# Kernel optimization log

Measured on AMD Instinct MI355X. Metric: run time of the kernel, lower is better.

The kernel has to match this reference:

```python
import jax, jax.numpy as jnp
import numpy as np

NA, NH, E, EL, D = 100000, 20000, 1000000, 200000, 128


def _sage(x_src, x_dst, src, dst, W_l, b_l, W_r, num_dst):
    # PyG SAGEConv: out = lin_l(mean_j x_src[j]) + lin_r(x_dst); lin_l has bias, lin_r does not.
    msg = x_src[src]                                   # [E, D] gather
    agg = jax.ops.segment_sum(msg, dst, num_segments=num_dst)   # [num_dst, D]
    deg = jax.ops.segment_sum(jnp.ones((src.shape[0],), x_src.dtype), dst, num_segments=num_dst)
    agg = agg / jnp.maximum(deg, 1.0)[:, None]         # mean aggregation; isolated nodes -> 0
    return agg @ W_l + b_l + x_dst @ W_r


def setup_inputs() -> dict:
    key = jax.random.key(0)
    ks = jax.random.split(key, 24)
    s = 1.0 / np.sqrt(D)
    inp = {
        "x_author": jax.random.normal(ks[0], (NA, D), jnp.float32),
        "x_hotel": jax.random.normal(ks[1], (NH, D), jnp.float32),
        "ei_ah_src": jax.random.randint(ks[2], (E,), 0, NA, jnp.int32),
        "ei_ah_dst": jax.random.randint(ks[3], (E,), 0, NH, jnp.int32),
        "ei_ha_src": jax.random.randint(ks[4], (E,), 0, NH, jnp.int32),
        "ei_ha_dst": jax.random.randint(ks[5], (E,), 0, NA, jnp.int32),
        "eli_row": jax.random.randint(ks[6], (EL,), 0, NA, jnp.int32),
        "eli_col": jax.random.randint(ks[7], (EL,), 0, NH, jnp.int32),
    }
    # per-layer, per-edge-type SAGE weights
    names = ["W1_ah_l", "W1_ah_r", "W1_ha_l", "W1_ha_r", "W2_ah_l", "W2_ah_r", "W2_ha_l", "W2_ha_r"]
    for i, n in enumerate(names):
        inp[n] = jax.random.normal(ks[8 + i], (D, D), jnp.float32) * s
    inp["b1_ah_l"] = jnp.zeros((D,), jnp.float32)
    inp["b1_ha_l"] = jnp.zeros((D,), jnp.float32)
    inp["b2_ah_l"] = jnp.zeros((D,), jnp.float32)
    inp["b2_ha_l"] = jnp.zeros((D,), jnp.float32)
    # decoder MLP
    inp["W_lin1"] = jax.random.normal(ks[16], (2 * D, D), jnp.float32) * (1.0 / np.sqrt(2 * D))
    inp["b_lin1"] = jnp.zeros((D,), jnp.float32)
    inp["W_lin2"] = jax.random.normal(ks[17], (D, 1), jnp.float32) * s
    inp["b_lin2"] = jnp.zeros((1,), jnp.float32)
    return inp


def reference(x_author, x_hotel, ei_ah_src, ei_ah_dst, ei_ha_src, ei_ha_dst,
              eli_row, eli_col,
              W1_ah_l, b1_ah_l, W1_ah_r, W1_ha_l, b1_ha_l, W1_ha_r,
              W2_ah_l, b2_ah_l, W2_ah_r, W2_ha_l, b2_ha_l, W2_ha_r,
              W_lin1, b_lin1, W_lin2, b_lin2):
    # layer 1 (HeteroConv: each node type receives from exactly one edge type) + relu
    h_hotel = jax.nn.relu(_sage(x_author, x_hotel, ei_ah_src, ei_ah_dst, W1_ah_l, b1_ah_l, W1_ah_r, NH))
    h_author = jax.nn.relu(_sage(x_hotel, x_author, ei_ha_src, ei_ha_dst, W1_ha_l, b1_ha_l, W1_ha_r, NA))
    # layer 2 (no relu on last layer)
    z_hotel = _sage(h_author, h_hotel, ei_ah_src, ei_ah_dst, W2_ah_l, b2_ah_l, W2_ah_r, NH)
    z_author = _sage(h_hotel, h_author, ei_ha_src, ei_ha_dst, W2_ha_l, b2_ha_l, W2_ha_r, NA)
    # edge decoder: gather-concat -> 2-layer MLP
    z1 = jnp.concatenate([z_author[eli_row], z_hotel[eli_col]], axis=-1)  # [EL, 2D]
    z2 = jax.nn.relu(z1 @ W_lin1 + b_lin1)                                # [EL, D]
    pred = (z2 @ W_lin2 + b_lin2).reshape(-1)                             # [EL]
    return (pred, z1, z2)
```

## Files before the change

kernel.cpp:

```cpp
#include <hip/hip_runtime.h>

#define NA_ 100000
#define NH_ 20000
#define E_  1000000
#define EL_ 200000
#define D_  128

typedef __attribute__((ext_vector_type(8))) short short8;
typedef __attribute__((ext_vector_type(4))) float f32x4;

__device__ __forceinline__ ushort f2bf(float f) {
  union { float f; uint u; } v; v.f = f;
  uint u = v.u;
  return (ushort)((u + 0x7FFFu + ((u >> 16) & 1u)) >> 16);
}
__device__ __forceinline__ uint pack2bf(float a, float b) {
  return (uint)f2bf(a) | ((uint)f2bf(b) << 16);
}


__global__ __launch_bounds__(256) void cvt_count_k(const float* __restrict__ xa, ushort* __restrict__ da,
                                                   const float* __restrict__ xh, ushort* __restrict__ dh,
                                                   const int* __restrict__ d1, int* __restrict__ c1,
                                                   const int* __restrict__ d2, int* __restrict__ c2) {
  int i = blockIdx.x * 256 + threadIdx.x;
  if (i < E_) atomicAdd(&c1[d1[i]], 1);
  else if (i < 2 * E_) atomicAdd(&c2[d2[i - E_]], 1);
  const int na4 = NA_ * 32;
  if (i < na4) {
    float4 v = *(const float4*)(xa + (size_t)i * 4);
    ((uint2*)da)[i] = make_uint2(pack2bf(v.x, v.y), pack2bf(v.z, v.w));
  } else {
    int k = i - na4;
    if (k < NH_ * 32) {
      float4 v = *(const float4*)(xh + (size_t)k * 4);
      ((uint2*)dh)[k] = make_uint2(pack2bf(v.x, v.y), pack2bf(v.z, v.w));
    }
  }
}


__global__ __launch_bounds__(1024) void scan2_k(int* __restrict__ c1, int* __restrict__ o1, int n1,
                                                int* __restrict__ c2, int* __restrict__ o2, int n2) {
  int* c = blockIdx.x ? c2 : c1;
  int* o = blockIdx.x ? o2 : o1;
  int n  = blockIdx.x ? n2 : n1;
  __shared__ int sums[1024];
  int t = threadIdx.x;
  int per = (n + 1023) >> 10;
  int s0 = t * per;
  int s1 = s0 + per; if (s1 > n) s1 = n;
  int loc = 0;
  for (int i = s0; i < s1; i++) loc += c[i];
  sums[t] = loc;
  __syncthreads();
  for (int sh = 1; sh < 1024; sh <<= 1) {
    int v = (t >= sh) ? sums[t - sh] : 0;
    __syncthreads();
    sums[t] += v;
    __syncthreads();
  }
  int run = (t == 0) ? 0 : sums[t - 1];
  for (int i = s0; i < s1; i++) {
    int ci = c[i];
    o[i] = run;
    c[i] = run;
    run += ci;
  }
  if (t == 1023) o[n] = run;
}

__global__ void fill_edges_k(const int* __restrict__ s1, const int* __restrict__ d1,
                             int* __restrict__ cur1, int* __restrict__ out1,
                             const int* __restrict__ s2, const int* __restrict__ d2,
                             int* __restrict__ cur2, int* __restrict__ out2) {
  int i = blockIdx.x * 256 + threadIdx.x;
  if (i < E_) {
    int p = atomicAdd(&cur1[d1[i]], 1);
    out1[p] = s1[i];
  } else if (i < 2 * E_) {
    int ii = i - E_;
    int p = atomicAdd(&cur2[d2[ii]], 1);
    out2[p] = s2[ii];
  }
}


__global__ void pack_all_k(const float* a0, const float* a1, ushort* ad,
                           const float* b0, const float* b1, ushort* bd,
                           const float* c0, const float* c1, ushort* cd,
                           const float* d0, const float* d1, ushort* dd,
                           const float* e0, const float* e1, ushort* ed) {
  const float *s0, *s1; ushort* dst;
  switch (blockIdx.y) {
    case 0: s0 = a0; s1 = a1; dst = ad; break;
    case 1: s0 = b0; s1 = b1; dst = bd; break;
    case 2: s0 = c0; s1 = c1; dst = cd; break;
    case 3: s0 = d0; s1 = d1; dst = dd; break;
    default: s0 = e0; s1 = e1; dst = ed; break;
  }
  int idx = blockIdx.x * 256 + threadIdx.x;
  int j = idx & 7, lane = (idx >> 3) & 63, nt = (idx >> 9) & 7, kc = idx >> 12;
  int k = kc * 32 + (lane >> 4) * 8 + j;
  int n = nt * 16 + (lane & 15);
  float v = (k < 128) ? s0[k * 128 + n] : s1[(k - 128) * 128 + n];
  dst[idx] = f2bf(v);
}


__global__ __launch_bounds__(256) void aggregate_bf_k(const ushort* __restrict__ xsrc,
                                                      const int* __restrict__ off,
                                                      const int* __restrict__ srcs,
                                                      ushort* __restrict__ out, int ndst) {
  int w = (blockIdx.x * 256 + threadIdx.x) >> 6;
  int lane = threadIdx.x & 63;
  if (w >= ndst) return;
  const int grp = lane >> 4, sub = lane & 15;
  int beg = off[w], end = off[w + 1];
  float a[8] = {0.f, 0.f, 0.f, 0.f, 0.f, 0.f, 0.f, 0.f};
  const ushort* base = xsrc + sub * 8;
  int j = beg + grp;
  for (; j + 4 < end; j += 8) {
    int sA = srcs[j];
    int sB = srcs[j + 4];
    uint4 vA = *(const uint4*)(base + (size_t)sA * 128);
    uint4 vB = *(const uint4*)(base + (size_t)sB * 128);
    a[0] += __uint_as_float(vA.x << 16); a[1] += __uint_as_float(vA.x & 0xFFFF0000u);
    a[2] += __uint_as_float(vA.y << 16); a[3] += __uint_as_float(vA.y & 0xFFFF0000u);
    a[4] += __uint_as_float(vA.z << 16); a[5] += __uint_as_float(vA.z & 0xFFFF0000u);
    a[6] += __uint_as_float(vA.w << 16); a[7] += __uint_as_float(vA.w & 0xFFFF0000u);
    a[0] += __uint_as_float(vB.x << 16); a[1] += __uint_as_float(vB.x & 0xFFFF0000u);
    a[2] += __uint_as_float(vB.y << 16); a[3] += __uint_as_float(vB.y & 0xFFFF0000u);
    a[4] += __uint_as_float(vB.z << 16); a[5] += __uint_as_float(vB.z & 0xFFFF0000u);
    a[6] += __uint_as_float(vB.w << 16); a[7] += __uint_as_float(vB.w & 0xFFFF0000u);
  }
  if (j < end) {
    int sA = srcs[j];
    uint4 vA = *(const uint4*)(base + (size_t)sA * 128);
    a[0] += __uint_as_float(vA.x << 16); a[1] += __uint_as_float(vA.x & 0xFFFF0000u);
    a[2] += __uint_as_float(vA.y << 16); a[3] += __uint_as_float(vA.y & 0xFFFF0000u);
    a[4] += __uint_as_float(vA.z << 16); a[5] += __uint_as_float(vA.z & 0xFFFF0000u);
    a[6] += __uint_as_float(vA.w << 16); a[7] += __uint_as_float(vA.w & 0xFFFF0000u);
  }
#pragma unroll
  for (int k = 0; k < 8; k++) {
    a[k] += __shfl_xor(a[k], 16);
    a[k] += __shfl_xor(a[k], 32);
  }
  int deg = end - beg;
  float sc = 1.0f / (float)(deg > 0 ? deg : 1);
  if (grp == 0) {
    uint4 o;
    o.x = pack2bf(a[0] * sc, a[1] * sc);
    o.y = pack2bf(a[2] * sc, a[3] * sc);
    o.z = pack2bf(a[4] * sc, a[5] * sc);
    o.w = pack2bf(a[6] * sc, a[7] * sc);
    *(uint4*)(out + (size_t)w * 128 + sub * 8) = o;
  }
}


template <bool RELU, bool OUTBF>
__global__ __launch_bounds__(256) void sage_mfma_k(const ushort* __restrict__ Abf,
                                                   const ushort* __restrict__ Xbf,
                                                   const ushort* __restrict__ Wp,
                                                   const float* __restrict__ bias,
                                                   float* __restrict__ outF,
                                                   ushort* __restrict__ outB, int rows) {
  const int t = threadIdx.x;
  const int w = t >> 6, lane = t & 63, quad = lane >> 4, m = lane & 15;
  const int row0 = blockIdx.x * 64 + w * 16;
  int rA = row0 + m; if (rA >= rows) rA = rows - 1;
  f32x4 acc[8];
#pragma unroll
  for (int nt = 0; nt < 8; nt++) acc[nt] = (f32x4){0.f, 0.f, 0.f, 0.f};
#pragma unroll
  for (int kc = 0; kc < 8; kc++) {
    const ushort* src = (kc < 4) ? (Abf + (size_t)rA * 128 + kc * 32)
                                 : (Xbf + (size_t)rA * 128 + (kc - 4) * 32);
    short8 a = *(const short8*)(src + quad * 8);
    const ushort* wp = Wp + (size_t)(kc * 8) * 512 + lane * 8;
#pragma unroll
    for (int nt = 0; nt < 8; nt++) {
      short8 b = *(const short8*)(wp + nt * 512);
      acc[nt] = __builtin_amdgcn_mfma_f32_16x16x32_bf16(a, b, acc[nt], 0, 0, 0);
    }
  }
#pragma unroll
  for (int nt = 0; nt < 8; nt++) {
    float bv = bias[nt * 16 + m];
#pragma unroll
    for (int r = 0; r < 4; r++) {
      int row = row0 + quad * 4 + r;
      if (row < rows) {
        float v = acc[nt][r] + bv;
        if (RELU) v = fmaxf(v, 0.f);
        if (OUTBF) outB[(size_t)row * 128 + nt * 16 + m] = f2bf(v);
        else       outF[(size_t)row * 128 + nt * 16 + m] = v;
      }
    }
  }
}


__global__ __launch_bounds__(256) void decoder_mfma_k(const float* __restrict__ Za,
                                                      const float* __restrict__ Zh,
                                                      const int* __restrict__ rowi,
                                                      const int* __restrict__ coli,
                                                      const ushort* __restrict__ Wp,
                                                      const float* __restrict__ b1,
                                                      const float* __restrict__ W2,
                                                      const float* __restrict__ b2,
                                                      float* __restrict__ pred,
                                                      float* __restrict__ z1o,
                                                      float* __restrict__ z2o) {
  __shared__ ushort z1bf[64 * 264];
  __shared__ int ra[64], rc[64];
  const int t = threadIdx.x, w = t >> 6, lane = t & 63, quad = lane >> 4, m = lane & 15;
  const int rb = blockIdx.x * 64;
  if (t < 64) ra[t] = rowi[rb + t];
  else if (t < 128) rc[t - 64] = coli[rb + t - 64];
  __syncthreads();
#pragma unroll 4
  for (int rr = 0; rr < 16; rr++) {
    int row = w * 16 + rr;
    int a = ra[row], c = rc[row];
    float2 va = *(const float2*)(Za + (size_t)a * 128 + lane * 2);
    float2 vc = *(const float2*)(Zh + (size_t)c * 128 + lane * 2);
    float* zr = z1o + (size_t)(rb + row) * 256;
    __builtin_nontemporal_store(*(const double*)&va, (double*)(zr + lane * 2));
    __builtin_nontemporal_store(*(const double*)&vc, (double*)(zr + 128 + lane * 2));
    uint* lbase = (uint*)(z1bf + row * 264);
    lbase[lane] = pack2bf(va.x, va.y);
    lbase[64 + lane] = pack2bf(vc.x, vc.y);
  }
  __syncthreads();
  f32x4 acc[8];
#pragma unroll
  for (int nt = 0; nt < 8; nt++) acc[nt] = (f32x4){0.f, 0.f, 0.f, 0.f};
#pragma unroll
  for (int kc = 0; kc < 8; kc++) {
    short8 a = *(const short8*)(z1bf + (w * 16 + m) * 264 + kc * 32 + quad * 8);
    const ushort* wp = Wp + (size_t)(kc * 8) * 512 + lane * 8;
#pragma unroll
    for (int nt = 0; nt < 8; nt++) {
      short8 b = *(const short8*)(wp + nt * 512);
      acc[nt] = __builtin_amdgcn_mfma_f32_16x16x32_bf16(a, b, acc[nt], 0, 0, 0);
    }
  }
  float part[4] = {0.f, 0.f, 0.f, 0.f};
#pragma unroll
  for (int nt = 0; nt < 8; nt++) {
    float bv = b1[nt * 16 + m];
    float wv = W2[nt * 16 + m];
#pragma unroll
    for (int r = 0; r < 4; r++) {
      float v = fmaxf(acc[nt][r] + bv, 0.f);
      __builtin_nontemporal_store(v, z2o + (size_t)(rb + w * 16 + quad * 4 + r) * 128 + nt * 16 + m);
      part[r] += v * wv;
    }
  }
  const float bias2 = b2[0];
#pragma unroll
  for (int r = 0; r < 4; r++) {
    float s = part[r];
    s += __shfl_xor(s, 1); s += __shfl_xor(s, 2);
    s += __shfl_xor(s, 4); s += __shfl_xor(s, 8);
    if (m == 0) pred[rb + w * 16 + quad * 4 + r] = s + bias2;
  }
}


static inline char* carve(char*& p, size_t bytes) {
  char* r = p;
  p += (bytes + 255) & ~(size_t)255;
  return r;
}

extern "C" void kernel_launch(void* const* d_in, const int* in_sizes, int n_in,
                              void* d_out, int out_size, void* d_ws, size_t ws_size,
                              hipStream_t stream) {
  const float* x_author = (const float*)d_in[0];
  const float* x_hotel  = (const float*)d_in[1];
  const int* ei_ah_src  = (const int*)d_in[2];
  const int* ei_ah_dst  = (const int*)d_in[3];
  const int* ei_ha_src  = (const int*)d_in[4];
  const int* ei_ha_dst  = (const int*)d_in[5];
  const int* eli_row    = (const int*)d_in[6];
  const int* eli_col    = (const int*)d_in[7];
  const float* W1_ah_l  = (const float*)d_in[8];
  const float* W1_ah_r  = (const float*)d_in[9];
  const float* W1_ha_l  = (const float*)d_in[10];
  const float* W1_ha_r  = (const float*)d_in[11];
  const float* W2_ah_l  = (const float*)d_in[12];
  const float* W2_ah_r  = (const float*)d_in[13];
  const float* W2_ha_l  = (const float*)d_in[14];
  const float* W2_ha_r  = (const float*)d_in[15];
  const float* b1_ah_l  = (const float*)d_in[16];
  const float* b1_ha_l  = (const float*)d_in[17];
  const float* b2_ah_l  = (const float*)d_in[18];
  const float* b2_ha_l  = (const float*)d_in[19];
  const float* W_lin1   = (const float*)d_in[20];
  const float* b_lin1   = (const float*)d_in[21];
  const float* W_lin2   = (const float*)d_in[22];
  const float* b_lin2   = (const float*)d_in[23];

  char* p = (char*)d_ws;
  ushort* xa_bf = (ushort*)carve(p, (size_t)NA_ * D_ * 2);
  ushort* xh_bf = (ushort*)carve(p, (size_t)NH_ * D_ * 2);
  ushort* A_hbf = (ushort*)carve(p, (size_t)NH_ * D_ * 2);
  ushort* A_abf = (ushort*)carve(p, (size_t)NA_ * D_ * 2);
  ushort* H_hbf = (ushort*)carve(p, (size_t)NH_ * D_ * 2);
  ushort* H_abf = (ushort*)carve(p, (size_t)NA_ * D_ * 2);
  float*  Z_h   = (float*)carve(p, (size_t)NH_ * D_ * 4);
  float*  Z_a   = (float*)carve(p, (size_t)NA_ * D_ * 4);
  ushort* Wp1ah = (ushort*)carve(p, 32768 * 2);
  ushort* Wp1ha = (ushort*)carve(p, 32768 * 2);
  ushort* Wp2ah = (ushort*)carve(p, 32768 * 2);
  ushort* Wp2ha = (ushort*)carve(p, 32768 * 2);
  ushort* WpD   = (ushort*)carve(p, 32768 * 2);
  int* off_h = (int*)carve(p, (size_t)(NH_ + 1) * 4);
  int* off_a = (int*)carve(p, (size_t)(NA_ + 1) * 4);
  int* cur_h = (int*)carve(p, (size_t)(NH_ + NA_) * 4);
  int* cur_a = cur_h + NH_;
  int* s_ah  = (int*)carve(p, (size_t)E_ * 4);
  int* s_ha  = (int*)carve(p, (size_t)E_ * 4);

  float* pred = (float*)d_out;
  float* z1o  = pred + EL_;
  float* z2o  = z1o + (size_t)EL_ * 256;

  hipMemsetAsync(cur_h, 0, (size_t)(NH_ + NA_) * 4, stream);
  cvt_count_k<<<(NA_ * 32 + NH_ * 32 + 255) / 256, 256, 0, stream>>>(
      x_author, xa_bf, x_hotel, xh_bf, ei_ah_dst, cur_h, ei_ha_dst, cur_a);
  scan2_k<<<2, 1024, 0, stream>>>(cur_h, off_h, NH_, cur_a, off_a, NA_);
  fill_edges_k<<<(2 * E_ + 255) / 256, 256, 0, stream>>>(ei_ah_src, ei_ah_dst, cur_h, s_ah,
                                                         ei_ha_src, ei_ha_dst, cur_a, s_ha);

  dim3 pg(128, 5);
  pack_all_k<<<pg, 256, 0, stream>>>(W1_ah_l, W1_ah_r, Wp1ah,
                                     W1_ha_l, W1_ha_r, Wp1ha,
                                     W2_ah_l, W2_ah_r, Wp2ah,
                                     W2_ha_l, W2_ha_r, Wp2ha,
                                     W_lin1, W_lin1 + 128 * 128, WpD);

  aggregate_bf_k<<<(NH_ + 3) / 4, 256, 0, stream>>>(xa_bf, off_h, s_ah, A_hbf, NH_);
  sage_mfma_k<true, true><<<(NH_ + 63) / 64, 256, 0, stream>>>(A_hbf, xh_bf, Wp1ah, b1_ah_l, nullptr, H_hbf, NH_);
  aggregate_bf_k<<<(NA_ + 3) / 4, 256, 0, stream>>>(xh_bf, off_a, s_ha, A_abf, NA_);
  sage_mfma_k<true, true><<<(NA_ + 63) / 64, 256, 0, stream>>>(A_abf, xa_bf, Wp1ha, b1_ha_l, nullptr, H_abf, NA_);

  aggregate_bf_k<<<(NH_ + 3) / 4, 256, 0, stream>>>(H_abf, off_h, s_ah, A_hbf, NH_);
  sage_mfma_k<false, false><<<(NH_ + 63) / 64, 256, 0, stream>>>(A_hbf, H_hbf, Wp2ah, b2_ah_l, Z_h, nullptr, NH_);
  aggregate_bf_k<<<(NA_ + 3) / 4, 256, 0, stream>>>(H_hbf, off_a, s_ha, A_abf, NA_);
  sage_mfma_k<false, false><<<(NA_ + 63) / 64, 256, 0, stream>>>(A_abf, H_abf, Wp2ha, b2_ha_l, Z_a, nullptr, NA_);

  decoder_mfma_k<<<EL_ / 64, 256, 0, stream>>>(Z_a, Z_h, eli_row, eli_col,
                                               WpD, b_lin1, W_lin2, b_lin2,
                                               pred, z1o, z2o);
}
```

Baseline: 1.099 ms.

## Replace two-block serial CSR scan with three-phase multi-block scan

The old offset scan ran on just two workgroups, with each thread walking about 100 counts serially, so it was latency bound. It is replaced by a reduce-then-scan-then-scatter pattern across 118 blocks using vectorized int4 loads and wave shuffles. This adds two extra kernel launches but spreads the scan across many compute units. The end offset is set to E directly, which assumes every edge is counted.

```diff
diff --git a/kernel.cpp b/kernel.cpp
--- a/kernel.cpp
+++ b/kernel.cpp
@@ -5,6 +5,10 @@
 #define E_  1000000
 #define EL_ 200000
 #define D_  128
+
+#define NBH_ 20
+#define NBA_ 98
+#define NBT_ 118
 
 typedef __attribute__((ext_vector_type(8))) short short8;
 typedef __attribute__((ext_vector_type(4))) float f32x4;
@@ -40,34 +44,99 @@
 }
 
 
-__global__ __launch_bounds__(1024) void scan2_k(int* __restrict__ c1, int* __restrict__ o1, int n1,
-                                                int* __restrict__ c2, int* __restrict__ o2, int n2) {
-  int* c = blockIdx.x ? c2 : c1;
-  int* o = blockIdx.x ? o2 : o1;
-  int n  = blockIdx.x ? n2 : n1;
-  __shared__ int sums[1024];
+__global__ __launch_bounds__(256) void csr_partial_k(const int* __restrict__ cnt_h,
+                                                     const int* __restrict__ cnt_a,
+                                                     int* __restrict__ partials) {
+  int b = blockIdx.x;
+  bool isH = b < NBH_;
+  const int* c = isH ? cnt_h : cnt_a;
+  int n = isH ? NH_ : NA_;
+  int chunk = isH ? b : b - NBH_;
   int t = threadIdx.x;
-  int per = (n + 1023) >> 10;
-  int s0 = t * per;
-  int s1 = s0 + per; if (s1 > n) s1 = n;
-  int loc = 0;
-  for (int i = s0; i < s1; i++) loc += c[i];
-  sums[t] = loc;
-  __syncthreads();
-  for (int sh = 1; sh < 1024; sh <<= 1) {
-    int v = (t >= sh) ? sums[t - sh] : 0;
+  int i0 = chunk * 1024 + t * 4;
+  int s = 0;
+  if (i0 + 3 < n) {
+    int4 v = *(const int4*)(c + i0);
+    s = v.x + v.y + v.z + v.w;
+  } else {
+    for (int k = 0; k < 4; k++) if (i0 + k < n) s += c[i0 + k];
+  }
+#pragma unroll
+  for (int d = 1; d < 64; d <<= 1) s += __shfl_xor(s, d);
+  __shared__ int ws[4];
+  int lane = t & 63, wv = t >> 6;
+  if (lane == 0) ws[wv] = s;
+  __syncthreads();
+  if (t == 0) partials[b] = ws[0] + ws[1] + ws[2] + ws[3];
+}
+
+
+__global__ __launch_bounds__(128) void csr_scanp_k(int* __restrict__ partials,
+                                                   int* __restrict__ off_h,
+                                                   int* __restrict__ off_a) {
+  __shared__ int s[128];
+  int t = threadIdx.x;
+  int orig = (t < NBT_) ? partials[t] : 0;
+  int seg = (t < NBH_) ? 0 : 1;
+  s[t] = orig;
+  __syncthreads();
+  for (int d = 1; d < 128; d <<= 1) {
+    int v = 0;
+    if (t >= d) {
+      int o = t - d;
+      if (((o < NBH_) ? 0 : 1) == seg) v = s[o];
+    }
     __syncthreads();
-    sums[t] += v;
+    s[t] += v;
     __syncthreads();
   }
-  int run = (t == 0) ? 0 : sums[t - 1];
-  for (int i = s0; i < s1; i++) {
-    int ci = c[i];
-    o[i] = run;
-    c[i] = run;
-    run += ci;
-  }
-  if (t == 1023) o[n] = run;
+  if (t < NBT_) partials[t] = s[t] - orig;
+  if (t == 0) { off_h[NH_] = E_; off_a[NA_] = E_; }
+}
+
+
+__global__ __launch_bounds__(256) void csr_scatter_k(int* __restrict__ cnt_h, int* __restrict__ off_h,
+                                                     int* __restrict__ cnt_a, int* __restrict__ off_a,
+                                                     const int* __restrict__ partials) {
+  int b = blockIdx.x;
+  bool isH = b < NBH_;
+  int* c = isH ? cnt_h : cnt_a;
+  int* off = isH ? off_h : off_a;
+  int n = isH ? NH_ : NA_;
+  int chunk = isH ? b : b - NBH_;
+  int t = threadIdx.x, lane = t & 63, wv = t >> 6;
+  int base = partials[b];
+  int i0 = chunk * 1024 + t * 4;
+  int v0 = 0, v1 = 0, v2 = 0, v3 = 0;
+  if (i0 + 3 < n) {
+    int4 v = *(const int4*)(c + i0);
+    v0 = v.x; v1 = v.y; v2 = v.z; v3 = v.w;
+  } else {
+    if (i0 < n) v0 = c[i0];
+    if (i0 + 1 < n) v1 = c[i0 + 1];
+    if (i0 + 2 < n) v2 = c[i0 + 2];
+    if (i0 + 3 < n) v3 = c[i0 + 3];
+  }
+  int tsum = v0 + v1 + v2 + v3;
+  int x = tsum;
+#pragma unroll
+  for (int d = 1; d < 64; d <<= 1) { int y = __shfl_up(x, d); if (lane >= d) x += y; }
+  __shared__ int ws[4], wb[4];
+  if (lane == 63) ws[wv] = x;
+  __syncthreads();
+  if (t == 0) { int r = 0; for (int i = 0; i < 4; i++) { wb[i] = r; r += ws[i]; } }
+  __syncthreads();
+  int run = base + wb[wv] + (x - tsum);
+  int o0 = run, o1 = o0 + v0, o2 = o1 + v1, o3 = o2 + v2;
+  if (i0 + 3 < n) {
+    *(int4*)(off + i0) = make_int4(o0, o1, o2, o3);
+    *(int4*)(c + i0) = make_int4(o0, o1, o2, o3);
+  } else {
+    if (i0 < n) { off[i0] = o0; c[i0] = o0; }
+    if (i0 + 1 < n) { off[i0 + 1] = o1; c[i0 + 1] = o1; }
+    if (i0 + 2 < n) { off[i0 + 2] = o2; c[i0 + 2] = o2; }
+    if (i0 + 3 < n) { off[i0 + 3] = o3; c[i0 + 3] = o3; }
+  }
 }
 
 __global__ void fill_edges_k(const int* __restrict__ s1, const int* __restrict__ d1,
@@ -325,6 +394,7 @@
   int* cur_a = cur_h + NH_;
   int* s_ah  = (int*)carve(p, (size_t)E_ * 4);
   int* s_ha  = (int*)carve(p, (size_t)E_ * 4);
+  int* partials = (int*)carve(p, 256 * 4);
 
   float* pred = (float*)d_out;
   float* z1o  = pred + EL_;
@@ -333,7 +403,11 @@
   hipMemsetAsync(cur_h, 0, (size_t)(NH_ + NA_) * 4, stream);
   cvt_count_k<<<(NA_ * 32 + NH_ * 32 + 255) / 256, 256, 0, stream>>>(
       x_author, xa_bf, x_hotel, xh_bf, ei_ah_dst, cur_h, ei_ha_dst, cur_a);
-  scan2_k<<<2, 1024, 0, stream>>>(cur_h, off_h, NH_, cur_a, off_a, NA_);
+
+  csr_partial_k<<<NBT_, 256, 0, stream>>>(cur_h, cur_a, partials);
+  csr_scanp_k<<<1, 128, 0, stream>>>(partials, off_h, off_a);
+  csr_scatter_k<<<NBT_, 256, 0, stream>>>(cur_h, off_h, cur_a, off_a, partials);
+
   fill_edges_k<<<(2 * E_ + 255) / 256, 256, 0, stream>>>(ei_ah_src, ei_ah_dst, cur_h, s_ah,
                                                          ei_ha_src, ei_ha_dst, cur_a, s_ha);
 
```

After: 904.9 us. 17.7% less time.
